# Kernel optimization log

Measured on AMD Instinct MI355X. Metric: run time of the kernel, lower is better.

Reference implementation:

```python
import jax, jax.numpy as jnp
import numpy as np

B, T, M, H = 256, 64, 256, 256


def setup_inputs() -> dict:
    key = jax.random.key(0)
    ks = jax.random.split(key, 16)
    n = jax.random.normal
    s = 0.05  # small init so tanh/sigmoid stay in sane range
    return {
        "enc_inputs": n(ks[0], (T, B, M), jnp.float32),  # module transposes (0,1) itself
        "y": n(ks[1], (B, T, 1), jnp.float32),
        "W_d": n(ks[2], (M, 2 * H), jnp.float32) * s,
        "b_Wd": n(ks[3], (M,), jnp.float32) * s,
        "U_d": n(ks[4], (M, M), jnp.float32) * s,
        "v_d": n(ks[5], (1, M), jnp.float32) * s,
        "w_tilda": n(ks[6], (1, M + 1), jnp.float32) * s,
        "b_wt": n(ks[7], (1,), jnp.float32) * s,
        "W_ih": n(ks[8], (4 * H, 1), jnp.float32) * s,
        "W_hh": n(ks[9], (4 * H, H), jnp.float32) * s,
        "b_ih": n(ks[10], (4 * H,), jnp.float32) * s,
        "b_hh": n(ks[11], (4 * H,), jnp.float32) * s,
        "W_y": n(ks[12], (H, H + M), jnp.float32) * s,
        "b_Wy": n(ks[13], (H,), jnp.float32) * s,
        "v_y": n(ks[14], (1, H), jnp.float32) * s,
        "b_vy": n(ks[15], (1,), jnp.float32) * s,
    }


def reference(enc_inputs, y, W_d, b_Wd, U_d, v_d, w_tilda, b_wt,
              W_ih, W_hh, b_ih, b_hh, W_y, b_Wy, v_y, b_vy):
    enc = jnp.swapaxes(enc_inputs, 0, 1)                 # (B,T,M)
    # U_d(enc) is loop-invariant; hoist (same math as recomputing per step)
    y1 = jnp.einsum('btm,nm->btn', enc, U_d)             # (B,T,M)
    ys = jnp.swapaxes(y, 0, 1)                           # (T,B,1) scanned over time
    b = enc.shape[0]
    d0 = jnp.zeros((b, H), enc.dtype)
    s0 = jnp.zeros((b, H), enc.dtype)
    c0 = jnp.zeros((b, M), enc.dtype)

    def step(carry, y_t):
        d, sp, _ = carry
        # Bahdanau-style temporal attention over encoder steps
        x1 = jnp.concatenate([d, sp], axis=1) @ W_d.T + b_Wd      # (B,M)
        l = jnp.tanh(x1[:, None, :] + y1) @ v_d[0]                # (B,T)
        beta = jax.nn.softmax(l, axis=1)
        c = jnp.einsum('bt,btm->bm', beta, enc)                   # (B,M)
        # scalar driving input for the decoder LSTM cell
        y_til = jnp.concatenate([c, y_t], axis=1) @ w_tilda.T + b_wt  # (B,1)
        # torch.nn.LSTMCell update with (h, c) = (d, sp)
        gates = y_til @ W_ih.T + b_ih + d @ W_hh.T + b_hh         # (B,4H)
        i, f, g, o = jnp.split(gates, 4, axis=1)
        sp_new = jax.nn.sigmoid(f) * sp + jax.nn.sigmoid(i) * jnp.tanh(g)
        d_new = jax.nn.sigmoid(o) * jnp.tanh(sp_new)
        return (d_new, sp_new, c), None

    (d, sp, c), _ = jax.lax.scan(step, (d0, s0, c0), ys)
    h = jnp.concatenate([d, c], axis=1) @ W_y.T + b_Wy            # (B,H)
    return h @ v_y.T + b_vy                                        # (B,1)
```

## Files before the change

### kernel.cpp

```cpp
#include <hip/hip_runtime.h>


#define Bx 256
#define Tx 64
#define Mx 256
#define Hx 256
#define NT 1024
#define XS 20

typedef unsigned int  uint;
typedef unsigned short ushort;
typedef _Float16 h2  __attribute__((ext_vector_type(2)));
typedef float    f2v __attribute__((ext_vector_type(2)));

__device__ __forceinline__ float4 ld4(const float* p) { return *(const float4*)p; }
__device__ __forceinline__ float h2f(ushort s) {
  union { ushort s; _Float16 h; } c; c.s = s; return (float)c.h;
}
__device__ __forceinline__ ushort f2h(float f) {
  union { _Float16 h; ushort s; } c; c.h = (_Float16)f; return c.s;
}
__device__ __forceinline__ uint pk2(float a, float b) {
  return (uint)f2h(a) | ((uint)f2h(b) << 16);
}
__device__ __forceinline__ float tanh_fast(float x) {
  float e2 = __expf(2.0f * x);
  return 1.0f - 2.0f / (e2 + 1.0f);
}
__device__ __forceinline__ float sigm(float x) {
  return 1.0f / (1.0f + __expf(-x));
}
__device__ __forceinline__ float wave_sum(float v) {
  #pragma unroll
  for (int o = 1; o < 64; o <<= 1) v += __shfl_xor(v, o, 64);
  return v;
}
__device__ __forceinline__ int xsw(int m) { return (m >> 4) * XS + (m & 15); }

#if defined(__has_builtin)
#if __has_builtin(__builtin_amdgcn_fdot2)
#define HAVE_FDOT2 1
#endif
#if __has_builtin(__builtin_amdgcn_cvt_pk_f32_fp8) && __has_builtin(__builtin_amdgcn_cvt_pk_fp8_f32)
#define HAVE_FP8 1
#endif
#endif

__device__ __forceinline__ float dot2u(uint w, uint a, float acc) {
#ifdef HAVE_FDOT2
  h2 W = __builtin_bit_cast(h2, w);
  h2 A = __builtin_bit_cast(h2, a);
  return __builtin_amdgcn_fdot2(W, A, acc, false);
#else
  return acc + h2f((ushort)w) * h2f((ushort)a)
             + h2f((ushort)(w >> 16)) * h2f((ushort)(a >> 16));
#endif
}

__device__ __forceinline__ uint sw8(float f) {
  union { float f; uint u; } c; c.f = f;
  uint s = (c.u >> 31) << 7;
  float a = fabsf(f);
  if (!(a >= 0.0009765625f)) return s;
  if (a >= 448.f) return s | 0x7e;
  int e = (int)((c.u >> 23) & 0xff) - 127;
  if (e < -6) { int q = (int)(a * 512.f + 0.5f); return s | (uint)q; }
  uint m = ((c.u & 0x7fffff) + 0x80000) >> 20;
  if (m == 8) { m = 0; ++e; }
  if (e > 8) return s | 0x7e;
  return s | ((uint)(e + 7) << 3) | m;
}
__device__ __forceinline__ float sw8d(uint b) {
  uint s = b >> 7, e = (b >> 3) & 0xf, m = b & 7;
  float v;
  if (e) { union { uint u; float f; } c; c.u = ((e + 120u) << 23) | (m << 20); v = c.f; }
  else v = (float)m * 0.001953125f;
  return s ? -v : v;
}
__device__ __forceinline__ uint pk_fp8x4(float w0, float w1, float w2, float w3) {
#ifdef HAVE_FP8
  int u = 0;
  u = __builtin_amdgcn_cvt_pk_fp8_f32(w0, w1, u, false);
  u = __builtin_amdgcn_cvt_pk_fp8_f32(w2, w3, u, true);
  return (uint)u;
#else
  return sw8(w0) | (sw8(w1) << 8) | (sw8(w2) << 16) | (sw8(w3) << 24);
#endif
}
template <bool HI>
__device__ __forceinline__ f2v dec2(uint w) {
#ifdef HAVE_FP8
  return __builtin_amdgcn_cvt_pk_f32_fp8((int)w, HI);
#else
  uint b0 = HI ? ((w >> 16) & 0xffu) : (w & 0xffu);
  uint b1 = HI ? (w >> 24) : ((w >> 8) & 0xffu);
  return f2v{sw8d(b0), sw8d(b1)};
#endif
}
__device__ __forceinline__ f2v dotq(uint w, float4 a, f2v acc) {
  acc += dec2<false>(w) * f2v{a.x, a.y};
  acc += dec2<true>(w)  * f2v{a.z, a.w};
  return acc;
}

__global__ __launch_bounds__(256)
void pack_weights(const float* __restrict__ W_d,
                  const float* __restrict__ W_hh,
                  const float* __restrict__ U_d,
                  const float* __restrict__ W_y,
                  uint4* __restrict__ Whh8q,
                  uint4* __restrict__ Wd8q,
                  uint4* __restrict__ Ud8,
                  float* __restrict__ Wyt) {
  const int blk = blockIdx.x, tid = threadIdx.x;
  if (blk < 16) {
    const int k16 = blk;
    #pragma unroll
    for (int q = 0; q < 4; ++q) {
      const int j = tid + 256 * q;
      const float* wr = W_hh + (size_t)j * 256 + 16 * k16;
      float4 a = ld4(wr), b = ld4(wr + 4), c = ld4(wr + 8), d = ld4(wr + 12);
      uint4 u;
      u.x = pk_fp8x4(16.f * a.x, 16.f * a.y, 16.f * a.z, 16.f * a.w);
      u.y = pk_fp8x4(16.f * b.x, 16.f * b.y, 16.f * b.z, 16.f * b.w);
      u.z = pk_fp8x4(16.f * c.x, 16.f * c.y, 16.f * c.z, 16.f * c.w);
      u.w = pk_fp8x4(16.f * d.x, 16.f * d.y, 16.f * d.z, 16.f * d.w);
      Whh8q[k16 * 1024 + j] = u;
    }
  } else if (blk < 48) {
    const int k16 = blk - 16;
    const float* wr = W_d + (size_t)tid * 512 + 16 * k16;
    float4 a = ld4(wr), b = ld4(wr + 4), c = ld4(wr + 8), d = ld4(wr + 12);
    uint4 u;
    u.x = pk_fp8x4(16.f * a.x, 16.f * a.y, 16.f * a.z, 16.f * a.w);
    u.y = pk_fp8x4(16.f * b.x, 16.f * b.y, 16.f * b.z, 16.f * b.w);
    u.z = pk_fp8x4(16.f * c.x, 16.f * c.y, 16.f * c.z, 16.f * c.w);
    u.w = pk_fp8x4(16.f * d.x, 16.f * d.y, 16.f * d.z, 16.f * d.w);
    Wd8q[k16 * 256 + tid] = u;
  } else if (blk < 80) {
    const int m8 = blk - 48;
    float4 a = ld4(U_d + (size_t)tid * 256 + 8 * m8);
    float4 b = ld4(U_d + (size_t)tid * 256 + 8 * m8 + 4);
    Ud8[m8 * 256 + tid] = uint4{pk2(a.x, a.y), pk2(a.z, a.w),
                                pk2(b.x, b.y), pk2(b.z, b.w)};
  } else {
    const int k0 = (blk - 80) * 4;
    float4 w = ld4(W_y + (size_t)tid * 512 + k0);
    Wyt[(k0 + 0) * 256 + tid] = w.x;
    Wyt[(k0 + 1) * 256 + tid] = w.y;
    Wyt[(k0 + 2) * 256 + tid] = w.z;
    Wyt[(k0 + 3) * 256 + tid] = w.w;
  }
}

__global__ __launch_bounds__(NT, 1)
void fused(const float* __restrict__ enc,
           const float* __restrict__ yv,
           const float* __restrict__ b_Wd,
           const float* __restrict__ v_d,
           const float* __restrict__ w_tilda,
           const float* __restrict__ b_wt,
           const float* __restrict__ W_ih,
           const float* __restrict__ b_ih,
           const float* __restrict__ b_hh,
           const float* __restrict__ b_Wy,
           const float* __restrict__ v_y,
           const float* __restrict__ b_vy,
           const uint4* __restrict__ Whh8q,
           const uint4* __restrict__ Wd8q,
           const uint4* __restrict__ Ud8,
           const float* __restrict__ Wyt,
           ushort* __restrict__ Y1,
           float* __restrict__ out)
{
  extern __shared__ __align__(16) uint4 wdl[];
  __shared__ __align__(16) float dsp_s[2 * Hx];
  __shared__ __align__(16) float xq_s[2 * 16 * XS];
  __shared__ __align__(16) float vd_s[16 * XS];
  __shared__ float gates_s[1024];
  __shared__ float dcfin_s[2 * Hx];
  __shared__ float l_s[Tx];
  __shared__ uint  beta2_s[Tx / 2];
  __shared__ float e_s[Tx];
  __shared__ float red_s[4];
  __shared__ float ytil_s;
  __shared__ unsigned flagX, flagL;

  const int b   = blockIdx.x;
  const int tid = threadIdx.x;
  const int h   = tid & 255;
  const int p   = tid >> 8;
  const size_t BM = (size_t)Bx * Mx;

  #pragma unroll
  for (int i = 0; i < 8; ++i) wdl[i * NT + tid] = Wd8q[i * NT + tid];
  if (tid < 256) vd_s[xsw(tid)] = v_d[tid];
  if (tid < 512) dsp_s[tid] = 0.0f;
  if (tid == 0) { flagX = 0u; flagL = 0u; }

  float bj0 = 0.f, bj1 = 0.f;
  if (tid < 512) { bj0 = b_ih[tid] + b_hh[tid]; bj1 = b_ih[tid + 512] + b_hh[tid + 512]; }
  float bWd_r = 0.f;
  if (tid >= 512 && tid < 768) bWd_r = b_Wd[tid - 512];
  float wih0 = 0.f, wih1 = 0.f, wih2 = 0.f, wih3 = 0.f;
  if (tid >= 512 && tid < 768) {
    const int hh = tid - 512;
    wih0 = W_ih[hh]; wih1 = W_ih[hh + 256]; wih2 = W_ih[hh + 512]; wih3 = W_ih[hh + 768];
  }
  float yv_r = 0.f;
  if (tid >= 512 && tid < 576) yv_r = yv[b * Tx + (tid - 512)];
  const float wty = w_tilda[Mx];
  const float bwt = b_wt[0];

  if (tid < Tx) {
    const float* er = enc + (size_t)tid * BM + (size_t)b * Mx;
    float acc = 0.0f;
    for (int m = 0; m < Mx; m += 4) {
      float4 e4 = ld4(er + m);
      float4 w4 = ld4(w_tilda + m);
      acc += e4.x * w4.x + e4.y * w4.y + e4.z * w4.z + e4.w * w4.w;
    }
    e_s[tid] = acc;
  }

  {
    const int n = h;
    const float* eb = enc + (size_t)b * Mx;
    for (int tb = p * 16; tb < p * 16 + 16; tb += 8) {
      f2v acc2[8];
      #pragma unroll
      for (int j = 0; j < 8; ++j) acc2[j] = f2v{0.f, 0.f};
      #pragma unroll 2
      for (int m8 = 0; m8 < 32; ++m8) {
        uint4 u = Ud8[m8 * 256 + n];
        f2v w01 = f2v{h2f((ushort)u.x), h2f((ushort)(u.x >> 16))};
        f2v w23 = f2v{h2f((ushort)u.y), h2f((ushort)(u.y >> 16))};
        f2v w45 = f2v{h2f((ushort)u.z), h2f((ushort)(u.z >> 16))};
        f2v w67 = f2v{h2f((ushort)u.w), h2f((ushort)(u.w >> 16))};
        #pragma unroll
        for (int j = 0; j < 8; ++j) {
          const float* ep = eb + (size_t)(tb + j) * BM + 8 * m8;
          float4 ea = ld4(ep), eb4 = ld4(ep + 4);
          acc2[j] += f2v{ea.x, ea.y} * w01;
          acc2[j] += f2v{ea.z, ea.w} * w23;
          acc2[j] += f2v{eb4.x, eb4.y} * w45;
          acc2[j] += f2v{eb4.z, eb4.w} * w67;
        }
      }
      #pragma unroll
      for (int j = 0; j < 8; ++j)
        Y1[((size_t)b * Tx + tb + j) * Mx + n] = f2h(acc2[j].x + acc2[j].y);
    }
  }
  __syncthreads();

  float sp_reg = 0.0f;

  for (int t = 0; t < Tx; ++t) {
    if (tid < 512) {
      f2v ga = f2v{0.f, 0.f}, gb = f2v{0.f, 0.f};
      const uint4* wp = Whh8q + tid;
      #pragma unroll 2
      for (int c = 0; c < 16; ++c) {
        uint4 wa = wp[c * 1024];
        uint4 wb = wp[c * 1024 + 512];
        const float4* ap = (const float4*)dsp_s + 4 * c;
        float4 a0 = ap[0], a1 = ap[1], a2 = ap[2], a3 = ap[3];
        ga = dotq(wa.x, a0, ga); ga = dotq(wa.y, a1, ga);
        ga = dotq(wa.z, a2, ga); ga = dotq(wa.w, a3, ga);
        gb = dotq(wb.x, a0, gb); gb = dotq(wb.y, a1, gb);
        gb = dotq(wb.z, a2, gb); gb = dotq(wb.w, a3, gb);
      }
      gates_s[tid]       = (ga.x + ga.y) * 0.0625f + bj0;
      gates_s[tid + 512] = (gb.x + gb.y) * 0.0625f + bj1;
    } else {
      const int idx = tid - 512;
      const int m = idx & 255, q = idx >> 8;
      const int tq = idx >> 3, lq = idx & 7;
      const ushort* y1r = Y1 + ((size_t)b * Tx + tq) * Mx + lq * 32;
      uint4 yq0 = *(const uint4*)(y1r);
      uint4 yq1 = *(const uint4*)(y1r + 8);
      uint4 yq2 = *(const uint4*)(y1r + 16);
      uint4 yq3 = *(const uint4*)(y1r + 24);
      {
        f2v xa2 = f2v{0.f, 0.f};
        const uint4* xp = wdl + m + (q * 16) * 256;
        #pragma unroll 4
        for (int i = 0; i < 16; ++i) {
          uint4 u = xp[i * 256];
          const float4* ap = (const float4*)dsp_s + 64 * q + 4 * i;
          float4 a0 = ap[0], a1 = ap[1], a2 = ap[2], a3 = ap[3];
          xa2 = dotq(u.x, a0, xa2); xa2 = dotq(u.y, a1, xa2);
          xa2 = dotq(u.z, a2, xa2); xa2 = dotq(u.w, a3, xa2);
        }
        xq_s[q * (16 * XS) + xsw(m)] = (xa2.x + xa2.y) * 0.0625f
                                     + (q == 0 ? bWd_r : 0.0f);
      }
      __threadfence_block();
      if ((threadIdx.x & 63) == 0)
        __hip_atomic_fetch_add(&flagX, 1u, __ATOMIC_RELEASE, __HIP_MEMORY_SCOPE_WORKGROUP);
      const unsigned tgtX = 8u * (unsigned)(t + 1);
      while (__hip_atomic_load(&flagX, __ATOMIC_ACQUIRE, __HIP_MEMORY_SCOPE_WORKGROUP) < tgtX) {}

      {
        float ps = 0.0f;
        uint yy[8] = {yq0.x, yq0.y, yq0.z, yq0.w, yq1.x, yq1.y, yq1.z, yq1.w};
        uint zz[8] = {yq2.x, yq2.y, yq2.z, yq2.w, yq3.x, yq3.y, yq3.z, yq3.w};
        #pragma unroll
        for (int g = 0; g < 8; ++g) {
          const int c   = 2 * lq + (g >> 2);
          const int off = c * XS + 4 * (g & 3);
          float4 xa0 = *(const float4*)(xq_s + off);
          float4 xa1 = *(const float4*)(xq_s + 16 * XS + off);
          float4 vv  = *(const float4*)(vd_s + off);
          uint ya = (g < 4) ? yy[2 * g] : zz[2 * (g - 4)];
          uint yb = (g < 4) ? yy[2 * g + 1] : zz[2 * (g - 4) + 1];
          ps += tanh_fast(xa0.x + xa1.x + h2f((ushort)ya)) * vv.x
              + tanh_fast(xa0.y + xa1.y + h2f((ushort)(ya >> 16))) * vv.y
              + tanh_fast(xa0.z + xa1.z + h2f((ushort)yb)) * vv.z
              + tanh_fast(xa0.w + xa1.w + h2f((ushort)(yb >> 16))) * vv.w;
        }
        ps += __shfl_xor(ps, 1, 64);
        ps += __shfl_xor(ps, 2, 64);
        ps += __shfl_xor(ps, 4, 64);
        if (lq == 0) l_s[tq] = ps;
      }
      __threadfence_block();
      if ((threadIdx.x & 63) == 0)
        __hip_atomic_fetch_add(&flagL, 1u, __ATOMIC_RELEASE, __HIP_MEMORY_SCOPE_WORKGROUP);

      if (idx < 64) {
        const unsigned tgtL = 8u * (unsigned)(t + 1);
        while (__hip_atomic_load(&flagL, __ATOMIC_ACQUIRE, __HIP_MEMORY_SCOPE_WORKGROUP) < tgtL) {}
        float v = l_s[idx];
        float mx = v;
        #pragma unroll
        for (int o = 1; o < 64; o <<= 1) mx = fmaxf(mx, __shfl_xor(mx, o, 64));
        float e = __expf(v - mx);
        float sm = e;
        #pragma unroll
        for (int o = 1; o < 64; o <<= 1) sm += __shfl_xor(sm, o, 64);
        float beta = e / sm;
        float bnext = __shfl_xor(beta, 1, 64);
        if ((idx & 1) == 0) beta2_s[idx >> 1] = pk2(beta, bnext);
        float term = beta * e_s[idx] + ((idx == t) ? (wty * yv_r + bwt) : 0.0f);
        float yt = wave_sum(term);
        if (idx == 0) ytil_s = yt;
      }
    }
    __syncthreads();

    if (tid >= 512 && tid < 768) {
      const int hh = tid - 512;
      const float ytil = ytil_s;
      float fi = sigm(gates_s[hh]       + ytil * wih0);
      float ff = sigm(gates_s[256 + hh] + ytil * wih1);
      float fg = tanh_fast(gates_s[512 + hh] + ytil * wih2);
      float fo = sigm(gates_s[768 + hh] + ytil * wih3);
      float spn = ff * sp_reg + fi * fg;
      float dn  = fo * tanh_fast(spn);
      sp_reg = spn;
      dsp_s[hh]       = dn;
      dsp_s[256 + hh] = spn;
      if (t == Tx - 1) dcfin_s[hh] = dn;
    }
    __syncthreads();
  }

  if (tid >= 512) {
    const int idx = tid - 512;
    const int m = idx >> 1, q = idx & 1;
    float acc = 0.0f;
    #pragma unroll 4
    for (int j = 0; j < 32; ++j) {
      const int tt = q * 32 + j;
      uint bp = beta2_s[tt >> 1];
      float bb = (tt & 1) ? h2f((ushort)(bp >> 16)) : h2f((ushort)bp);
      acc += bb * enc[(size_t)tt * BM + (size_t)b * Mx + m];
    }
    acc += __shfl_xor(acc, 1, 64);
    if (q == 0) dcfin_s[256 + m] = acc;
  }
  __syncthreads();

  {
    float a = 0.0f;
    const float* wy = Wyt + h;
    for (int k = 128 * p; k < 128 * p + 128; ++k)
      a += wy[(size_t)k * 256] * dcfin_s[k];
    gates_s[p * 256 + h] = a;
  }
  __syncthreads();
  if (tid < 256) {
    float aa = gates_s[h] + gates_s[256 + h] + gates_s[512 + h] + gates_s[768 + h]
             + b_Wy[h];
    float po = aa * v_y[h];
    po = wave_sum(po);
    if ((tid & 63) == 0) red_s[tid >> 6] = po;
  }
  __syncthreads();
  if (tid == 0) out[b] = red_s[0] + red_s[1] + red_s[2] + red_s[3] + b_vy[0];
}

extern "C" void kernel_launch(void* const* d_in, const int* in_sizes, int n_in,
                              void* d_out, int out_size, void* d_ws, size_t ws_size,
                              hipStream_t stream) {
  const float* enc     = (const float*)d_in[0];
  const float* yv      = (const float*)d_in[1];
  const float* W_d     = (const float*)d_in[2];
  const float* b_Wd    = (const float*)d_in[3];
  const float* U_d     = (const float*)d_in[4];
  const float* v_d     = (const float*)d_in[5];
  const float* w_tilda = (const float*)d_in[6];
  const float* b_wt    = (const float*)d_in[7];
  const float* W_ih    = (const float*)d_in[8];
  const float* W_hh    = (const float*)d_in[9];
  const float* b_ih    = (const float*)d_in[10];
  const float* b_hh    = (const float*)d_in[11];
  const float* W_y     = (const float*)d_in[12];
  const float* b_Wy    = (const float*)d_in[13];
  const float* v_y     = (const float*)d_in[14];
  const float* b_vy    = (const float*)d_in[15];
  float* outp = (float*)d_out;

  char* ws = (char*)d_ws;
  uint4* Whh8q = (uint4*)ws;
  uint4* Wd8q  = (uint4*)(ws + (256 << 10));
  uint4* Ud8   = (uint4*)(ws + (384 << 10));
  float* Wyt   = (float*)(ws + (512 << 10));
  ushort* Y1   = (ushort*)(ws + (1024 << 10));

  const int DYN_LDS = 128 << 10;
  hipFuncSetAttribute((const void*)fused,
                      hipFuncAttributeMaxDynamicSharedMemorySize, DYN_LDS);

  hipLaunchKernelGGL(pack_weights, dim3(208), dim3(256), 0, stream,
                     W_d, W_hh, U_d, W_y, Whh8q, Wd8q, Ud8, Wyt);
  hipLaunchKernelGGL(fused, dim3(Bx), dim3(NT), DYN_LDS, stream,
                     enc, yv, b_Wd, v_d, w_tilda, b_wt, W_ih, b_ih, b_hh,
                     b_Wy, v_y, b_vy, Whh8q, Wd8q, Ud8, Wyt, Y1, outp);
}
```

Baseline: 702.5 us.

## Rebalance weight residency across LDS and registers, keep Y1 in LDS, simplify softmax

Moves the W_d chunk from LDS into per-thread registers and uses the freed LDS to hold part of W_hh plus the per-batch Y1 (U_d·enc) tile, so the recurrent loop no longer rereads Y1 or all of W_hh from global memory each step. The global W_hh chunks are prefetched two steps ahead in a software pipeline. The softmax drops the max-subtraction and computes y_tilde directly from the numerator and denominator sums, materialising beta only on the final step. It also swaps divisions for hardware reciprocals. Risks include more register pressure from 16 uint4 weight registers per thread and possible overflow, since the exponent is no longer max-shifted.

Measured after the change: 821.1 us. 1.17x slower.

```diff
diff --git a/kernel.cpp b/kernel.cpp
--- a/kernel.cpp
+++ b/kernel.cpp
@@ -7,6 +7,9 @@
 #define Hx 256
 #define NT 1024
 #define XS 20
+#define Y1R 264
+#define WCH_LDS 7
+#define WCH_STR 9
 
 typedef unsigned int  uint;
 typedef unsigned short ushort;
@@ -23,12 +26,28 @@
 __device__ __forceinline__ uint pk2(float a, float b) {
   return (uint)f2h(a) | ((uint)f2h(b) << 16);
 }
+
+#if defined(__has_builtin)
+#if __has_builtin(__builtin_amdgcn_rcpf)
+#define RCPF(x) __builtin_amdgcn_rcpf(x)
+#endif
+#if __has_builtin(__builtin_amdgcn_fdot2)
+#define HAVE_FDOT2 1
+#endif
+#if __has_builtin(__builtin_amdgcn_cvt_pk_f32_fp8) && __has_builtin(__builtin_amdgcn_cvt_pk_fp8_f32)
+#define HAVE_FP8 1
+#endif
+#endif
+#ifndef RCPF
+#define RCPF(x) (1.0f / (x))
+#endif
+
 __device__ __forceinline__ float tanh_fast(float x) {
   float e2 = __expf(2.0f * x);
-  return 1.0f - 2.0f / (e2 + 1.0f);
+  return 1.0f - 2.0f * RCPF(e2 + 1.0f);
 }
 __device__ __forceinline__ float sigm(float x) {
-  return 1.0f / (1.0f + __expf(-x));
+  return RCPF(1.0f + __expf(-x));
 }
 __device__ __forceinline__ float wave_sum(float v) {
   #pragma unroll
@@ -36,15 +55,6 @@
   return v;
 }
 __device__ __forceinline__ int xsw(int m) { return (m >> 4) * XS + (m & 15); }
-
-#if defined(__has_builtin)
-#if __has_builtin(__builtin_amdgcn_fdot2)
-#define HAVE_FDOT2 1
-#endif
-#if __has_builtin(__builtin_amdgcn_cvt_pk_f32_fp8) && __has_builtin(__builtin_amdgcn_cvt_pk_fp8_f32)
-#define HAVE_FP8 1
-#endif
-#endif
 
 __device__ __forceinline__ float dot2u(uint w, uint a, float acc) {
 #ifdef HAVE_FDOT2
@@ -170,10 +180,12 @@
            const uint4* __restrict__ Wd8q,
            const uint4* __restrict__ Ud8,
            const float* __restrict__ Wyt,
-           ushort* __restrict__ Y1,
            float* __restrict__ out)
 {
-  extern __shared__ __align__(16) uint4 wdl[];
+  extern __shared__ __align__(16) char dyn[];
+  uint4*  whl  = (uint4*)dyn;
+  ushort* y1_s = (ushort*)(dyn + WCH_LDS * 1024 * 16);
+
   __shared__ __align__(16) float dsp_s[2 * Hx];
   __shared__ __align__(16) float xq_s[2 * 16 * XS];
   __shared__ __align__(16) float vd_s[16 * XS];
@@ -193,7 +205,8 @@
   const size_t BM = (size_t)Bx * Mx;
 
   #pragma unroll
-  for (int i = 0; i < 8; ++i) wdl[i * NT + tid] = Wd8q[i * NT + tid];
+  for (int i = 0; i < WCH_LDS; ++i)
+    whl[i * 1024 + tid] = Whh8q[(WCH_STR + i) * 1024 + tid];
   if (tid < 256) vd_s[xsw(tid)] = v_d[tid];
   if (tid < 512) dsp_s[tid] = 0.0f;
   if (tid == 0) { flagX = 0u; flagL = 0u; }
@@ -249,8 +262,15 @@
       }
       #pragma unroll
       for (int j = 0; j < 8; ++j)
-        Y1[((size_t)b * Tx + tb + j) * Mx + n] = f2h(acc2[j].x + acc2[j].y);
-    }
+        y1_s[(size_t)(tb + j) * Y1R + n] = f2h(acc2[j].x + acc2[j].y);
+    }
+  }
+
+  uint4 wdr[16];
+  if (tid >= 512) {
+    const int mm = (tid - 512) & 255, qq = (tid - 512) >> 8;
+    #pragma unroll
+    for (int i = 0; i < 16; ++i) wdr[i] = Wd8q[(qq * 16 + i) * 256 + mm];
   }
   __syncthreads();
 
@@ -258,12 +278,14 @@
 
   for (int t = 0; t < Tx; ++t) {
     if (tid < 512) {
+      const uint4* wp = Whh8q + tid;
+      uint4 pa = wp[0],    pb = wp[512];
+      uint4 qa = wp[1024], qb = wp[1024 + 512];
       f2v ga = f2v{0.f, 0.f}, gb = f2v{0.f, 0.f};
-      const uint4* wp = Whh8q + tid;
-      #pragma unroll 2
-      for (int c = 0; c < 16; ++c) {
-        uint4 wa = wp[c * 1024];
-        uint4 wb = wp[c * 1024 + 512];
+      #pragma unroll
+      for (int c = WCH_STR; c < 16; ++c) {
+        uint4 wa = whl[(c - WCH_STR) * 1024 + tid];
+        uint4 wb = whl[(c - WCH_STR) * 1024 + tid + 512];
         const float4* ap = (const float4*)dsp_s + 4 * c;
         float4 a0 = ap[0], a1 = ap[1], a2 = ap[2], a3 = ap[3];
         ga = dotq(wa.x, a0, ga); ga = dotq(wa.y, a1, ga);
@@ -271,23 +293,28 @@
         gb = dotq(wb.x, a0, gb); gb = dotq(wb.y, a1, gb);
         gb = dotq(wb.z, a2, gb); gb = dotq(wb.w, a3, gb);
       }
+      #pragma unroll
+      for (int c = 0; c < WCH_STR; ++c) {
+        uint4 wa = pa, wb = pb; pa = qa; pb = qb;
+        if (c < WCH_STR - 2) { qa = wp[(c + 2) * 1024]; qb = wp[(c + 2) * 1024 + 512]; }
+        const float4* ap = (const float4*)dsp_s + 4 * c;
+        float4 a0 = ap[0], a1 = ap[1], a2 = ap[2], a3 = ap[3];
+        ga = dotq(wa.x, a0, ga); ga = dotq(wa.y, a1, ga);
+        ga = dotq(wa.z, a2, ga); ga = dotq(wa.w, a3, ga);
+        gb = dotq(wb.x, a0, gb); gb = dotq(wb.y, a1, gb);
+        gb = dotq(wb.z, a2, gb); gb = dotq(wb.w, a3, gb);
+      }
       gates_s[tid]       = (ga.x + ga.y) * 0.0625f + bj0;
       gates_s[tid + 512] = (gb.x + gb.y) * 0.0625f + bj1;
     } else {
       const int idx = tid - 512;
       const int m = idx & 255, q = idx >> 8;
       const int tq = idx >> 3, lq = idx & 7;
-      const ushort* y1r = Y1 + ((size_t)b * Tx + tq) * Mx + lq * 32;
-      uint4 yq0 = *(const uint4*)(y1r);
-      uint4 yq1 = *(const uint4*)(y1r + 8);
-      uint4 yq2 = *(const uint4*)(y1r + 16);
-      uint4 yq3 = *(const uint4*)(y1r + 24);
       {
         f2v xa2 = f2v{0.f, 0.f};
-        const uint4* xp = wdl + m + (q * 16) * 256;
-        #pragma unroll 4
+        #pragma unroll
         for (int i = 0; i < 16; ++i) {
-          uint4 u = xp[i * 256];
+          uint4 u = wdr[i];
           const float4* ap = (const float4*)dsp_s + 64 * q + 4 * i;
           float4 a0 = ap[0], a1 = ap[1], a2 = ap[2], a3 = ap[3];
           xa2 = dotq(u.x, a0, xa2); xa2 = dotq(u.y, a1, xa2);
@@ -303,6 +330,11 @@
       while (__hip_atomic_load(&flagX, __ATOMIC_ACQUIRE, __HIP_MEMORY_SCOPE_WORKGROUP) < tgtX) {}
 
       {
+        const ushort* y1r = y1_s + tq * Y1R + lq * 32;
+        uint4 yq0 = *(const uint4*)(y1r);
+        uint4 yq1 = *(const uint4*)(y1r + 8);
+        uint4 yq2 = *(const uint4*)(y1r + 16);
+        uint4 yq3 = *(const uint4*)(y1r + 24);
         float ps = 0.0f;
         uint yy[8] = {yq0.x, yq0.y, yq0.z, yq0.w, yq1.x, yq1.y, yq1.z, yq1.w};
         uint zz[8] = {yq2.x, yq2.y, yq2.z, yq2.w, yq3.x, yq3.y, yq3.z, yq3.w};
@@ -332,20 +364,20 @@
       if (idx < 64) {
         const unsigned tgtL = 8u * (unsigned)(t + 1);
         while (__hip_atomic_load(&flagL, __ATOMIC_ACQUIRE, __HIP_MEMORY_SCOPE_WORKGROUP) < tgtL) {}
-        float v = l_s[idx];
-        float mx = v;
+        float e0  = __expf(l_s[idx]);
+        float den = e0;
+        float num = e0 * e_s[idx];
         #pragma unroll
-        for (int o = 1; o < 64; o <<= 1) mx = fmaxf(mx, __shfl_xor(mx, o, 64));
-        float e = __expf(v - mx);
-        float sm = e;
-        #pragma unroll
-        for (int o = 1; o < 64; o <<= 1) sm += __shfl_xor(sm, o, 64);
-        float beta = e / sm;
-        float bnext = __shfl_xor(beta, 1, 64);
-        if ((idx & 1) == 0) beta2_s[idx >> 1] = pk2(beta, bnext);
-        float term = beta * e_s[idx] + ((idx == t) ? (wty * yv_r + bwt) : 0.0f);
-        float yt = wave_sum(term);
-        if (idx == 0) ytil_s = yt;
+        for (int o = 1; o < 64; o <<= 1) {
+          den += __shfl_xor(den, o, 64);
+          num += __shfl_xor(num, o, 64);
+        }
+        if (t == Tx - 1) {
+          float beta = e0 * RCPF(den);
+          float bn = __shfl_xor(beta, 1, 64);
+          if (!(idx & 1)) beta2_s[idx >> 1] = pk2(beta, bn);
+        }
+        if (idx == t) ytil_s = num * RCPF(den) + wty * yv_r + bwt;
       }
     }
     __syncthreads();
@@ -428,9 +460,8 @@
   uint4* Wd8q  = (uint4*)(ws + (256 << 10));
   uint4* Ud8   = (uint4*)(ws + (384 << 10));
   float* Wyt   = (float*)(ws + (512 << 10));
-  ushort* Y1   = (ushort*)(ws + (1024 << 10));
-
-  const int DYN_LDS = 128 << 10;
+
+  const int DYN_LDS = WCH_LDS * 1024 * 16 + Tx * Y1R * 2;
   hipFuncSetAttribute((const void*)fused,
                       hipFuncAttributeMaxDynamicSharedMemorySize, DYN_LDS);
 
@@ -438,5 +469,5 @@
                      W_d, W_hh, U_d, W_y, Whh8q, Wd8q, Ud8, Wyt);
   hipLaunchKernelGGL(fused, dim3(Bx), dim3(NT), DYN_LDS, stream,
                      enc, yv, b_Wd, v_d, w_tilda, b_wt, W_ih, b_ih, b_hh,
-                     b_Wy, v_y, b_vy, Whh8q, Wd8q, Ud8, Wyt, Y1, outp);
-}
+                     b_Wy, v_y, b_vy, Whh8q, Wd8q, Ud8, Wyt, outp);
+}
```
